# Kernel optimization log

Hardware: AMD Instinct MI355X
Metric: run time of the kernel (lower is better)

The kernel has to match this reference:

```python
import jax, jax.numpy as jnp
from jax import lax
import numpy as np

KAPPA_S = 6.0
KAPPA_D = 5.0
POLICY_STRETCH = 2.0
VALUE_STRETCH = 1.0 / 32.0
VALUE_GAUGE = 0.2

RAW_PATTERNS = [
    [[0, 0, 0, 0, -5, 1, 1, 1, 1], [0, 0, 0, 0, -5, -5, -5, -5, -5], 0],
    [[0, 0, 0, 1, -5, 1, 1, 1, 0], [0, 0, 0, -5, -5, -5, -5, -5, 0], 0],
    [[0, 0, 1, 1, -5, 1, 1, 0, 0], [0, 0, -5, -5, -5, -5, -5, 0, 0], 0],
    [[0, 1, 1, 1, -5, 1, 0, 0, 0], [0, -5, -5, -5, -5, -5, 0, 0, 0], 0],
    [[1, 1, 1, 1, -5, 0, 0, 0, 0], [-5, -5, -5, -5, -5, 0, 0, 0, 0], 0],
    [[0, -5, 1, 1, 1, 1, 1, -5, 0], [0, 0, -5, -5, -5, -5, -5, 0, 0], -4],
]


def _all_3xnxn(p3):
    # Lay a 9-long 1D pattern (one per input channel) along the 4 line
    # directions (horizontal, vertical, two diagonals) of a 9x9 kernel.
    f = np.zeros((9, 9, 3, 4), np.float32)
    for ch in range(3):
        v = np.asarray(p3[ch], np.float32)
        f[4, :, ch, 0] = v                       # horizontal
        f[:, 4, ch, 1] = v                       # vertical
        for i in range(9):
            f[i, i, ch, 2] = v[i]                # main diagonal
            f[i, 8 - i, ch, 3] = v[i]            # anti diagonal
    return f


def _assemble_filters():
    # select_patterns: channel 0 -> [offense, defense, defense]; channel 1 -> [defense, offense, defense]
    patterns = []
    for off, de, bias in RAW_PATTERNS:
        patterns.append(([off, de, de], bias))
        patterns.append(([de, off, de], bias))
    filt = np.stack([_all_3xnxn(p) for p, _ in patterns], axis=3)  # (9,9,3,12,4)
    filt = np.reshape(filt, (9, 9, 3, -1))                          # filter idx = 4*pattern + direction
    biases = np.asarray([b for _, b in patterns for _ in range(4)], np.float32)
    return jnp.asarray(filt), jnp.asarray(biases)


def _safe_pow(x, p):
    # x >= 0 everywhere it is used; guards the grad of x**p (p<1) at x==0.
    pos = x > 0
    return jnp.where(pos, jnp.where(pos, x, 1.0) ** p, 0.0)


def setup_inputs() -> dict:
    key = jax.random.key(0)
    state = jax.random.normal(key, (4096, 19, 19, 3), dtype=jnp.float32)
    W, b = _assemble_filters()
    return {"state": state, "W": W, "b": b}


def reference(state, W, b):
    # detector: Conv2D 9x9, 48 filters, SAME padding, relu
    counts = jax.nn.relu(
        lax.conv_general_dilated(
            state, W, window_strides=(1, 1), padding="SAME",
            dimension_numbers=("NHWC", "HWIO", "NHWC"),
        ) + b
    )  # [B, N, N, 48]
    # peel: 3x3 conv with identity-center kernel, VALID padding == crop of 1
    core = counts[:, 1:-1, 1:-1, :]  # [B, N-2, N-2, 48]
    B, H, Wd, _ = core.shape
    # filter index = 8*shift + 4*channel + direction for the 40 line filters
    core40 = core[..., :40].reshape(B, H, Wd, 5, 2, 4)  # (shift, channel, direction)
    s = jnp.sum(core40 ** KAPPA_S, axis=3)               # sum over shifts -> [B,H,W,2,4]
    sd = jnp.sum(_safe_pow(s, KAPPA_D / KAPPA_S), axis=4)  # sum over directions -> [B,H,W,2]
    f = _safe_pow(sd, 1.0 / KAPPA_D)                     # [B,H,W,2]; [...,c] = field(channel c)
    f_cur, f_oth = f[..., 0], f[..., 1]
    logits = (f_cur + f_oth).reshape(B, -1)
    probs = jax.nn.softmax(POLICY_STRETCH * logits, axis=-1)
    raw_value = VALUE_GAUGE * (jnp.sum(f_cur, axis=(1, 2)) - jnp.sum(f_oth, axis=(1, 2)))
    value = jnp.tanh(VALUE_STRETCH * raw_value)
    return probs, value
```

## Files before the change

kernel.cpp:

```cpp
#include <hip/hip_runtime.h>
#include <math.h>


__device__ __forceinline__ float fpow(float x, float e) {
    float r = __builtin_amdgcn_exp2f(e * __builtin_amdgcn_logf(x));
    return (x > 0.f) ? r : 0.f;
}
__device__ __forceinline__ float fexp(float x) {
    return __builtin_amdgcn_exp2f(x * 1.44269504088896f);
}

__global__ __launch_bounds__(256) void topo_policy_value(
    const float* __restrict__ state,
    float* __restrict__ probs,
    float* __restrict__ value)
{
    __shared__ float lin[3][27][27];
    __shared__ float red[12];

    const int tid = threadIdx.x;
    const int b = blockIdx.x;

    float* lz = &lin[0][0][0];
    #pragma unroll
    for (int i = 0; i < 9; ++i) {
        int idx = tid + i * 256;
        if (idx < 3 * 27 * 27) lz[idx] = 0.0f;
    }
    __syncthreads();

    const float* src = state + (size_t)b * (19 * 19 * 3);
    for (int j = tid; j < 19 * 19 * 3; j += 256) {
        float v = src[j];
        int y = j / 57;
        int r = j - y * 57;
        int x = r / 3;
        int c = r - x * 3;
        lin[c][y + 4][x + 4] = v;
    }
    __syncthreads();

    float fc[2] = {0.f, 0.f};
    float fo[2] = {0.f, 0.f};

    #pragma unroll
    for (int it = 0; it < 2; ++it) {
        const int pos = tid + it * 256;
        if (pos < 289) {
            const int y = pos / 17;
            const int x = pos - y * 17;

            float s0[4], s1[4];
            #pragma unroll
            for (int o = 0; o < 4; ++o) { s0[o] = 0.f; s1[o] = 0.f; }

            #pragma unroll
            for (int o = 0; o < 4; ++o) {
                float L0[9], L1[9], L2[9];
                #pragma unroll
                for (int i = 0; i < 9; ++i) {
                    int yy, xx;
                    if (o == 0)      { yy = y + 5;     xx = x + 1 + i; }
                    else if (o == 1) { yy = y + 1 + i; xx = x + 5;     }
                    else if (o == 2) { yy = y + 1 + i; xx = x + 1 + i; }
                    else             { yy = y + 1 + i; xx = x + 9 - i; }
                    L0[i] = lin[0][yy][xx];
                    L1[i] = lin[1][yy][xx];
                    L2[i] = lin[2][yy][xx];
                }
                float w0 = L0[4] + L0[5] + L0[6] + L0[7] + L0[8];
                float w1 = L1[4] + L1[5] + L1[6] + L1[7] + L1[8];
                float w2 = L2[4] + L2[5] + L2[6] + L2[7] + L2[8];
                const float C0 = L0[4], C1 = L1[4];
                #pragma unroll
                for (int p = 0; p < 5; ++p) {
                    float t  = w0 + w1 + w2;
                    float a0 = 6.f * (w0 - C0) - 5.f * t;
                    float a1 = 6.f * (w1 - C1) - 5.f * t;
                    a0 = fmaxf(a0, 0.f);
                    a1 = fmaxf(a1, 0.f);
                    float q0 = a0 * a0, q1 = a1 * a1;
                    s0[o] += q0 * q0 * q0;
                    s1[o] += q1 * q1 * q1;
                    if (p < 4) {
                        w0 += L0[3 - p] - L0[8 - p];
                        w1 += L1[3 - p] - L1[8 - p];
                        w2 += L2[3 - p] - L2[8 - p];
                    }
                }
            }
            float sd0 = 0.f, sd1 = 0.f;
            #pragma unroll
            for (int o = 0; o < 4; ++o) {
                sd0 += fpow(s0[o], 5.0f / 6.0f);
                sd1 += fpow(s1[o], 5.0f / 6.0f);
            }
            fc[it] = fpow(sd0, 0.2f);
            fo[it] = fpow(sd1, 0.2f);
        }
    }

    const bool act1 = (tid + 256) < 289;
    const float g0 = 2.f * (fc[0] + fo[0]);
    const float g1 = act1 ? 2.f * (fc[1] + fo[1]) : -3.0e38f;
    float lmax = fmaxf(g0, g1);
    float ldif = (fc[0] - fo[0]) + (fc[1] - fo[1]);

    #pragma unroll
    for (int off = 32; off > 0; off >>= 1) {
        lmax = fmaxf(lmax, __shfl_down(lmax, off, 64));
        ldif += __shfl_down(ldif, off, 64);
    }
    const int wave = tid >> 6;
    if ((tid & 63) == 0) { red[wave] = lmax; red[4 + wave] = ldif; }
    __syncthreads();
    if (tid == 0) {
        red[8] = fmaxf(fmaxf(red[0], red[1]), fmaxf(red[2], red[3]));
        red[9] = red[4] + red[5] + red[6] + red[7];
    }
    __syncthreads();

    const float M = red[8];
    const float e0 = fexp(g0 - M);
    const float e1 = act1 ? fexp(g1 - M) : 0.f;
    float lsum = e0 + e1;
    #pragma unroll
    for (int off = 32; off > 0; off >>= 1) lsum += __shfl_down(lsum, off, 64);
    if ((tid & 63) == 0) red[wave] = lsum;
    __syncthreads();
    if (tid == 0) red[10] = red[0] + red[1] + red[2] + red[3];
    __syncthreads();

    const float invS = 1.0f / red[10];
    float* pout = probs + (size_t)b * 289;
    pout[tid] = e0 * invS;
    if (act1) pout[tid + 256] = e1 * invS;
    if (tid == 0) value[b] = tanhf(red[9] * (0.2f / 32.0f));
}

extern "C" void kernel_launch(void* const* d_in, const int* in_sizes, int n_in,
                              void* d_out, int out_size, void* d_ws, size_t ws_size,
                              hipStream_t stream) {
    const float* state = (const float*)d_in[0];
    const int nb = in_sizes[0] / (19 * 19 * 3);
    float* probs = (float*)d_out;
    float* value = probs + (size_t)nb * 289;
    topo_policy_value<<<dim3(nb), dim3(256), 0, stream>>>(state, probs, value);
}
```

Before: 94.62 us.

## Precompute per-line 5-window sums in LDS instead of per-position sliding windows

Folds the channel combination into two precomputed per-pixel values (e0 = l0 - 5(l1+l2), e1 likewise) and a centre term, then runs one sliding 5-window sum along each line of every direction, storing it in shared memory. Each output position then needs only 5 LDS reads per direction and channel, instead of 27 reads and running sums per direction. This adds an extra phase in which only 200 of the 256 threads each do serial prefix-style scans, plus an extra barrier and more shared memory per block.

Result: faster. 86.06 us (-9.1%).

```diff
diff --git a/kernel.cpp b/kernel.cpp
--- a/kernel.cpp
+++ b/kernel.cpp
@@ -10,33 +10,91 @@
     return __builtin_amdgcn_exp2f(x * 1.44269504088896f);
 }
 
+#define OFF_E0 0
+#define OFF_E1 729
+#define OFF_C0 1458
+#define OFF_C1 1747
+#define OFF_GH 2036
+#define OFF_GV 2750
+#define OFF_GD 3464
+#define OFF_GA 4916
+#define LDS_FLOATS 6302
+
 __global__ __launch_bounds__(256) void topo_policy_value(
     const float* __restrict__ state,
     float* __restrict__ probs,
     float* __restrict__ value)
 {
-    __shared__ float lin[3][27][27];
+    __shared__ float lds[LDS_FLOATS];
     __shared__ float red[12];
 
     const int tid = threadIdx.x;
     const int b = blockIdx.x;
 
-    float* lz = &lin[0][0][0];
     #pragma unroll
-    for (int i = 0; i < 9; ++i) {
+    for (int i = 0; i < 6; ++i) {
         int idx = tid + i * 256;
-        if (idx < 3 * 27 * 27) lz[idx] = 0.0f;
+        if (idx < 1458) lds[idx] = 0.0f;
     }
     __syncthreads();
 
     const float* src = state + (size_t)b * (19 * 19 * 3);
-    for (int j = tid; j < 19 * 19 * 3; j += 256) {
-        float v = src[j];
-        int y = j / 57;
-        int r = j - y * 57;
-        int x = r / 3;
-        int c = r - x * 3;
-        lin[c][y + 4][x + 4] = v;
+    #pragma unroll
+    for (int it = 0; it < 2; ++it) {
+        int j = tid + it * 256;
+        if (j < 361) {
+            int br = j / 19, bc = j - br * 19;
+            float l0 = src[3 * j], l1 = src[3 * j + 1], l2 = src[3 * j + 2];
+            float e0 = fmaf(-5.f, l1 + l2, l0);
+            float e1 = fmaf(-5.f, l0 + l2, l1);
+            int pi = (br + 4) * 27 + (bc + 4);
+            lds[OFF_E0 + pi] = e0;
+            lds[OFF_E1 + pi] = e1;
+            if (br >= 1 && br <= 17 && bc >= 1 && bc <= 17) {
+                int ci = (br - 1) * 17 + (bc - 1);
+                lds[OFF_C0 + ci] = 6.f * l0;
+                lds[OFF_C1 + ci] = 6.f * l1;
+            }
+        }
+    }
+    __syncthreads();
+
+    if (tid < 200) {
+        int t = tid, f, L;
+        int base, step, outp, cnt;
+        if (t < 34) {
+            f = t & 1; L = t >> 1;
+            base = (L + 5) * 27 + 1; step = 1;
+            outp = OFF_GH + f * 357 + L * 21; cnt = 21;
+        } else if (t < 68) {
+            t -= 34; f = t & 1; L = t >> 1;
+            base = 27 + (L + 5); step = 27;
+            outp = OFF_GV + f * 357 + L * 21; cnt = 21;
+        } else if (t < 134) {
+            t -= 68; f = t & 1; L = t >> 1;
+            int d = L - 16;
+            int j0 = (d < 0) ? -d : 0;
+            base = (j0 + 1 + d) * 27 + (j0 + 1); step = 28;
+            outp = OFF_GD + f * 726 + L * 22 + j0;
+            cnt = 21 - ((d < 0) ? -d : d);
+        } else {
+            t -= 134; f = t & 1; L = t >> 1;
+            int k0 = (L > 16) ? (L - 16) : 0;
+            int k1 = (L + 4 < 20) ? (L + 4) : 20;
+            base = 26 * k0 + 36 + L; step = 26;
+            outp = OFF_GA + f * 693 + L * 21 + k0;
+            cnt = k1 - k0 + 1;
+        }
+        const float* ef = lds + ((f == 0) ? OFF_E0 : OFF_E1);
+        float s = ef[base] + ef[base + step] + ef[base + 2 * step]
+                + ef[base + 3 * step] + ef[base + 4 * step];
+        lds[outp] = s;
+        int lo = base, hi = base + 5 * step;
+        for (int i = 1; i < cnt; ++i) {
+            s += ef[hi] - ef[lo];
+            lo += step; hi += step;
+            lds[outp + i] = s;
+        }
     }
     __syncthreads();
 
@@ -49,52 +107,36 @@
         if (pos < 289) {
             const int y = pos / 17;
             const int x = pos - y * 17;
+            const float h0 = lds[OFF_C0 + pos];
+            const float h1 = lds[OFF_C1 + pos];
 
-            float s0[4], s1[4];
-            #pragma unroll
-            for (int o = 0; o < 4; ++o) { s0[o] = 0.f; s1[o] = 0.f; }
+            const int bh = OFF_GH + y * 21 + x;
+            const int bv = OFF_GV + x * 21 + y;
+            const int bd = OFF_GD + (y - x + 16) * 22 + x;
+            const int ba = OFF_GA + (y + x) * 21 + y;
 
-            #pragma unroll
-            for (int o = 0; o < 4; ++o) {
-                float L0[9], L1[9], L2[9];
-                #pragma unroll
-                for (int i = 0; i < 9; ++i) {
-                    int yy, xx;
-                    if (o == 0)      { yy = y + 5;     xx = x + 1 + i; }
-                    else if (o == 1) { yy = y + 1 + i; xx = x + 5;     }
-                    else if (o == 2) { yy = y + 1 + i; xx = x + 1 + i; }
-                    else             { yy = y + 1 + i; xx = x + 9 - i; }
-                    L0[i] = lin[0][yy][xx];
-                    L1[i] = lin[1][yy][xx];
-                    L2[i] = lin[2][yy][xx];
-                }
-                float w0 = L0[4] + L0[5] + L0[6] + L0[7] + L0[8];
-                float w1 = L1[4] + L1[5] + L1[6] + L1[7] + L1[8];
-                float w2 = L2[4] + L2[5] + L2[6] + L2[7] + L2[8];
-                const float C0 = L0[4], C1 = L1[4];
-                #pragma unroll
-                for (int p = 0; p < 5; ++p) {
-                    float t  = w0 + w1 + w2;
-                    float a0 = 6.f * (w0 - C0) - 5.f * t;
-                    float a1 = 6.f * (w1 - C1) - 5.f * t;
-                    a0 = fmaxf(a0, 0.f);
-                    a1 = fmaxf(a1, 0.f);
-                    float q0 = a0 * a0, q1 = a1 * a1;
-                    s0[o] += q0 * q0 * q0;
-                    s1[o] += q1 * q1 * q1;
-                    if (p < 4) {
-                        w0 += L0[3 - p] - L0[8 - p];
-                        w1 += L1[3 - p] - L1[8 - p];
-                        w2 += L2[3 - p] - L2[8 - p];
-                    }
-                }
+            float sd0 = 0.f, sd1 = 0.f;
+            #define ORIENT(B, FS)                                         \
+            {                                                             \
+                float t0 = 0.f, t1 = 0.f;                                 \
+                _Pragma("unroll")                                         \
+                for (int i = 0; i < 5; ++i) {                             \
+                    float a0 = lds[(B) + i] - h0;                         \
+                    float a1 = lds[(B) + (FS) + i] - h1;                  \
+                    a0 = fmaxf(a0, 0.f); a1 = fmaxf(a1, 0.f);             \
+                    float q0 = a0 * a0, q1 = a1 * a1;                     \
+                    float m0 = q0 * q0, m1 = q1 * q1;                     \
+                    t0 = fmaf(m0, q0, t0); t1 = fmaf(m1, q1, t1);         \
+                }                                                         \
+                sd0 += fpow(t0, 5.0f / 6.0f);                             \
+                sd1 += fpow(t1, 5.0f / 6.0f);                             \
             }
-            float sd0 = 0.f, sd1 = 0.f;
-            #pragma unroll
-            for (int o = 0; o < 4; ++o) {
-                sd0 += fpow(s0[o], 5.0f / 6.0f);
-                sd1 += fpow(s1[o], 5.0f / 6.0f);
-            }
+            ORIENT(bh, 357)
+            ORIENT(bv, 357)
+            ORIENT(bd, 726)
+            ORIENT(ba, 693)
+            #undef ORIENT
+
             fc[it] = fpow(sd0, 0.2f);
             fo[it] = fpow(sd1, 0.2f);
         }
```

## Process one board per wavefront with pre-combined channel planes in LDS

Applied to the files above, without the earlier changes.

Each 64-lane wavefront now handles a whole board, so four boards share a 256-thread block and all block-wide __syncthreads and LDS reductions become wave shuffles. The three input planes are pre-combined in LDS into two float2 line-sum terms (offense minus five times defense) plus a 6x center term. This cuts the per-position arithmetic and the number of LDS reads. Each lane now computes up to five positions instead of one or two, and tanh and the reciprocal use hardware approximations, which raises per-thread work and register pressure and may slightly change accuracy.

New measurement: 84.84 us. -10.3%, faster.

```diff
diff --git a/kernel.cpp b/kernel.cpp
--- a/kernel.cpp
+++ b/kernel.cpp
@@ -10,132 +10,131 @@
     return __builtin_amdgcn_exp2f(x * 1.44269504088896f);
 }
 
+#define SLAB 1024
+#define C_OFF 729
+
 __global__ __launch_bounds__(256) void topo_policy_value(
     const float* __restrict__ state,
     float* __restrict__ probs,
-    float* __restrict__ value)
+    float* __restrict__ value,
+    int nb)
 {
-    __shared__ float lin[3][27][27];
-    __shared__ float red[12];
+    __shared__ float2 l2[4 * SLAB];
 
-    const int tid = threadIdx.x;
-    const int b = blockIdx.x;
-
-    float* lz = &lin[0][0][0];
-    #pragma unroll
-    for (int i = 0; i < 9; ++i) {
-        int idx = tid + i * 256;
-        if (idx < 3 * 27 * 27) lz[idx] = 0.0f;
-    }
-    __syncthreads();
+    const int tid  = threadIdx.x;
+    const int wv   = tid >> 6;
+    const int lane = tid & 63;
+    const int b    = blockIdx.x * 4 + wv;
+    if (b >= nb) return;
+    float2* s2 = l2 + wv * SLAB;
 
     const float* src = state + (size_t)b * (19 * 19 * 3);
-    for (int j = tid; j < 19 * 19 * 3; j += 256) {
-        float v = src[j];
-        int y = j / 57;
-        int r = j - y * 57;
-        int x = r / 3;
-        int c = r - x * 3;
-        lin[c][y + 4][x + 4] = v;
-    }
-    __syncthreads();
-
-    float fc[2] = {0.f, 0.f};
-    float fo[2] = {0.f, 0.f};
 
     #pragma unroll
-    for (int it = 0; it < 2; ++it) {
-        const int pos = tid + it * 256;
-        if (pos < 289) {
-            const int y = pos / 17;
-            const int x = pos - y * 17;
-
-            float s0[4], s1[4];
-            #pragma unroll
-            for (int o = 0; o < 4; ++o) { s0[o] = 0.f; s1[o] = 0.f; }
-
-            #pragma unroll
-            for (int o = 0; o < 4; ++o) {
-                float L0[9], L1[9], L2[9];
-                #pragma unroll
-                for (int i = 0; i < 9; ++i) {
-                    int yy, xx;
-                    if (o == 0)      { yy = y + 5;     xx = x + 1 + i; }
-                    else if (o == 1) { yy = y + 1 + i; xx = x + 5;     }
-                    else if (o == 2) { yy = y + 1 + i; xx = x + 1 + i; }
-                    else             { yy = y + 1 + i; xx = x + 9 - i; }
-                    L0[i] = lin[0][yy][xx];
-                    L1[i] = lin[1][yy][xx];
-                    L2[i] = lin[2][yy][xx];
-                }
-                float w0 = L0[4] + L0[5] + L0[6] + L0[7] + L0[8];
-                float w1 = L1[4] + L1[5] + L1[6] + L1[7] + L1[8];
-                float w2 = L2[4] + L2[5] + L2[6] + L2[7] + L2[8];
-                const float C0 = L0[4], C1 = L1[4];
-                #pragma unroll
-                for (int p = 0; p < 5; ++p) {
-                    float t  = w0 + w1 + w2;
-                    float a0 = 6.f * (w0 - C0) - 5.f * t;
-                    float a1 = 6.f * (w1 - C1) - 5.f * t;
-                    a0 = fmaxf(a0, 0.f);
-                    a1 = fmaxf(a1, 0.f);
-                    float q0 = a0 * a0, q1 = a1 * a1;
-                    s0[o] += q0 * q0 * q0;
-                    s1[o] += q1 * q1 * q1;
-                    if (p < 4) {
-                        w0 += L0[3 - p] - L0[8 - p];
-                        w1 += L1[3 - p] - L1[8 - p];
-                        w2 += L2[3 - p] - L2[8 - p];
-                    }
-                }
+    for (int it = 0; it < 12; ++it) {
+        int j = lane + it * 64;
+        if (j < 729) {
+            int py = j / 27, px = j - py * 27;
+            int r = py - 4, c = px - 4;
+            float l0 = 0.f, l1 = 0.f, lv = 0.f;
+            if ((unsigned)r < 19u && (unsigned)c < 19u) {
+                int o = 3 * (r * 19 + c);
+                l0 = src[o]; l1 = src[o + 1]; lv = src[o + 2];
             }
-            float sd0 = 0.f, sd1 = 0.f;
-            #pragma unroll
-            for (int o = 0; o < 4; ++o) {
-                sd0 += fpow(s0[o], 5.0f / 6.0f);
-                sd1 += fpow(s1[o], 5.0f / 6.0f);
-            }
-            fc[it] = fpow(sd0, 0.2f);
-            fo[it] = fpow(sd1, 0.2f);
+            s2[j] = make_float2(fmaf(-5.f, l1 + lv, l0),
+                                fmaf(-5.f, l0 + lv, l1));
         }
     }
+    #pragma unroll
+    for (int it = 0; it < 5; ++it) {
+        int j = lane + it * 64;
+        if (j < 289) {
+            int y = j / 17, x = j - y * 17;
+            int o = 3 * ((y + 1) * 19 + (x + 1));
+            s2[C_OFF + j] = make_float2(6.f * src[o], 6.f * src[o + 1]);
+        }
+    }
+    __builtin_amdgcn_s_waitcnt(0);
+    __builtin_amdgcn_wave_barrier();
 
-    const bool act1 = (tid + 256) < 289;
-    const float g0 = 2.f * (fc[0] + fo[0]);
-    const float g1 = act1 ? 2.f * (fc[1] + fo[1]) : -3.0e38f;
-    float lmax = fmaxf(g0, g1);
-    float ldif = (fc[0] - fo[0]) + (fc[1] - fo[1]);
+    float g[5], es[5];
+    float dif = 0.f;
+    #pragma unroll
+    for (int k = 0; k < 5; ++k) {
+        int p = lane + 64 * k;
+        float gk = -3.0e38f;
+        if (p < 289) {
+            int y = p / 17, x = p - y * 17;
+            float2 h = s2[C_OFF + p];
+            int c0 = (y + 5) * 27 + (x + 1);
+            int c1 = (y + 1) * 27 + (x + 5);
+            int c2 = (y + 1) * 27 + (x + 1);
+            int c3 = (y + 1) * 27 + (x + 9);
+            float sd0 = 0.f, sd1 = 0.f;
+            #define ORIENT(BASE, STEP)                                      \
+            {                                                               \
+                float2 e[9];                                                \
+                _Pragma("unroll")                                           \
+                for (int i = 0; i < 9; ++i) e[i] = s2[(BASE) + i * (STEP)]; \
+                float wx = e[4].x + e[5].x + e[6].x + e[7].x + e[8].x;      \
+                float wy = e[4].y + e[5].y + e[6].y + e[7].y + e[8].y;      \
+                float t0 = 0.f, t1 = 0.f;                                   \
+                _Pragma("unroll")                                           \
+                for (int pp = 0; pp < 5; ++pp) {                            \
+                    float a0 = fmaxf(wx - h.x, 0.f);                        \
+                    float a1 = fmaxf(wy - h.y, 0.f);                        \
+                    float q0 = a0 * a0, q1 = a1 * a1;                       \
+                    t0 = fmaf(q0 * q0, q0, t0);                             \
+                    t1 = fmaf(q1 * q1, q1, t1);                             \
+                    if (pp < 4) {                                           \
+                        wx += e[3 - pp].x - e[8 - pp].x;                    \
+                        wy += e[3 - pp].y - e[8 - pp].y;                    \
+                    }                                                       \
+                }                                                           \
+                sd0 += fpow(t0, 5.0f / 6.0f);                               \
+                sd1 += fpow(t1, 5.0f / 6.0f);                               \
+            }
+            ORIENT(c0, 1)
+            ORIENT(c1, 27)
+            ORIENT(c2, 28)
+            ORIENT(c3, 26)
+            #undef ORIENT
+            float fc = fpow(sd0, 0.2f);
+            float fo = fpow(sd1, 0.2f);
+            gk = 2.f * (fc + fo);
+            dif += fc - fo;
+        }
+        g[k] = gk;
+    }
 
+    float M = fmaxf(fmaxf(fmaxf(g[0], g[1]), fmaxf(g[2], g[3])), g[4]);
     #pragma unroll
-    for (int off = 32; off > 0; off >>= 1) {
-        lmax = fmaxf(lmax, __shfl_down(lmax, off, 64));
-        ldif += __shfl_down(ldif, off, 64);
+    for (int off = 32; off > 0; off >>= 1)
+        M = fmaxf(M, __shfl_xor(M, off, 64));
+
+    float S = 0.f;
+    #pragma unroll
+    for (int k = 0; k < 5; ++k) {
+        es[k] = (g[k] > -1.0e38f) ? fexp(g[k] - M) : 0.f;
+        S += es[k];
     }
-    const int wave = tid >> 6;
-    if ((tid & 63) == 0) { red[wave] = lmax; red[4 + wave] = ldif; }
-    __syncthreads();
-    if (tid == 0) {
-        red[8] = fmaxf(fmaxf(red[0], red[1]), fmaxf(red[2], red[3]));
-        red[9] = red[4] + red[5] + red[6] + red[7];
+    #pragma unroll
+    for (int off = 32; off > 0; off >>= 1) S += __shfl_xor(S, off, 64);
+    #pragma unroll
+    for (int off = 32; off > 0; off >>= 1) dif += __shfl_xor(dif, off, 64);
+
+    const float invS = __builtin_amdgcn_rcpf(S);
+    float* pout = probs + (size_t)b * 289;
+    #pragma unroll
+    for (int k = 0; k < 5; ++k) {
+        int p = lane + 64 * k;
+        if (p < 289) pout[p] = es[k] * invS;
     }
-    __syncthreads();
-
-    const float M = red[8];
-    const float e0 = fexp(g0 - M);
-    const float e1 = act1 ? fexp(g1 - M) : 0.f;
-    float lsum = e0 + e1;
-    #pragma unroll
-    for (int off = 32; off > 0; off >>= 1) lsum += __shfl_down(lsum, off, 64);
-    if ((tid & 63) == 0) red[wave] = lsum;
-    __syncthreads();
-    if (tid == 0) red[10] = red[0] + red[1] + red[2] + red[3];
-    __syncthreads();
-
-    const float invS = 1.0f / red[10];
-    float* pout = probs + (size_t)b * 289;
-    pout[tid] = e0 * invS;
-    if (act1) pout[tid + 256] = e1 * invS;
-    if (tid == 0) value[b] = tanhf(red[9] * (0.2f / 32.0f));
+    if (lane == 0) {
+        float z = dif * (0.2f / 32.0f);
+        float t = __builtin_amdgcn_exp2f(z * (2.0f * 1.44269504088896f));
+        value[b] = (t - 1.f) * __builtin_amdgcn_rcpf(t + 1.f);
+    }
 }
 
 extern "C" void kernel_launch(void* const* d_in, const int* in_sizes, int n_in,
@@ -145,5 +144,6 @@
     const int nb = in_sizes[0] / (19 * 19 * 3);
     float* probs = (float*)d_out;
     float* value = probs + (size_t)nb * 289;
-    topo_policy_value<<<dim3(nb), dim3(256), 0, stream>>>(state, probs, value);
+    const int grid = (nb + 3) / 4;
+    topo_policy_value<<<dim3(grid), dim3(256), 0, stream>>>(state, probs, value, nb);
 }
```
